# Kernel optimization log

Measured on AMD Instinct MI355X. Metric: run time of the kernel, lower is better.

Reference implementation:

```python
import jax, jax.numpy as jnp
import numpy as np

# GCK basis vectors: all palindromic, so convolution == correlation for them.
_V = np.array([[1., 1., 1.], [1., -1., 1.], [1., 1., -1.]], dtype=np.float32)


def _lin_combs(kernels):
    """Coefficients c s.t. each 3x3 kernel = sum_k c_k * (v_i outer v_j), k=i*3+j.
    kernels: (O, C, 3, 3) -> (O, C*9), matching torch linCombs layout."""
    O, C = kernels.shape[0], kernels.shape[1]
    basis_flat = jnp.asarray(np.kron(_V, _V))           # (9, 9), symmetric
    basis_inv = jnp.linalg.inv(basis_flat)              # 9x9, tiny
    w = kernels.reshape(O, C, 9)
    comb = jnp.einsum('kl,ocl->ock', basis_inv, w)      # (O, C, 9)
    return comb.reshape(O, C * 9)


def setup_inputs() -> dict:
    key = jax.random.key(0)
    k1, k2 = jax.random.split(key)
    C_in, C_out, D = 16, 32, 1024
    x = jax.random.normal(k1, (C_in, D + 2, D + 2), dtype=jnp.float32)
    kernels = jax.random.normal(k2, (C_out, C_in, 3, 3), dtype=jnp.float32)
    return {"x": x, "kernels": kernels}


def reference(x, kernels):
    V = jnp.asarray(_V, dtype=x.dtype)
    lin = _lin_combs(kernels)                                   # (O, C*9)
    O = kernels.shape[0]
    C, H, W = x.shape
    D = H - 2  # result_dim (square image)
    # rowwise pass: 3-tap 'box' filters along height -> (C, 3, D, W)
    rw = jnp.stack([x[:, :-2, :], x[:, 1:-1, :], x[:, 2:, :]], axis=0)  # (3, C, D, W)
    rw = jnp.einsum('ir,rchw->cihw', V, rw)                              # (C, 3, D, W)
    # colwise pass: 3-tap filters along width -> (C, 3, 3, D, D)
    cw = jnp.stack([rw[..., :-2], rw[..., 1:-1], rw[..., 2:]], axis=0)   # (3, C, 3, D, D)
    cw = jnp.einsum('js,scihw->cijhw', V, cw)                            # (C, 3, 3, D, D)
    # final per-output-channel linear combination of the 9 basis responses
    cw = cw.reshape(C * 9, D * D)
    out = lin @ cw                                                       # (O, D*D)
    return out.reshape(O, D, D)
```

## Files before the change

### kernel.cpp

```cpp
#include <hip/hip_runtime.h>

typedef __attribute__((ext_vector_type(8))) short short8;
typedef __attribute__((ext_vector_type(16))) float f32x16;
typedef __attribute__((ext_vector_type(2))) float f32x2;
typedef __attribute__((ext_vector_type(4))) float f32x4u __attribute__((aligned(4)));
typedef __attribute__((ext_vector_type(2))) unsigned int uint2v;

#define C_INPUT 16
#define C_OUTPUT 32
#define DIM 1024
#define HW 1026
#define CH_STRIDE (HW * HW)
#define TH 16
#define TW 32
#define LDS_ROWS 18
#define LDS_W 34
#define ROW_BYTES (LDS_W * 32)
#define LDS_BYTES (LDS_ROWS * ROW_BYTES)
#define NUNITS (4 * LDS_ROWS * 9)

__device__ __forceinline__ unsigned short f2bf(float f) {
    unsigned int u = __builtin_bit_cast(unsigned int, f);
    u += 0x7fffu + ((u >> 16) & 1u);
    return (unsigned short)(u >> 16);
}

__global__ __launch_bounds__(256, 4)
void gck3x3_mfma_kernel(const float* __restrict__ x,
                        const float* __restrict__ kern,
                        float* __restrict__ out) {
    __shared__ __attribute__((aligned(16))) unsigned char s_x[LDS_BYTES];

    const int tid  = threadIdx.x;
    const int lane = tid & 63;
    const int wv   = tid >> 6;
    const int n    = lane & 31;
    const int hi   = lane >> 5;

    const int bid = blockIdx.x;
    const int swz = (bid & 7) * 256 + (bid >> 3);
    const int bh  = swz >> 5;
    const int bw  = swz & 31;
    const int h0  = bh * TH;
    const int w0  = bw * TW;

    f32x4u vals[3][4];
    #pragma unroll
    for (int k = 0; k < 3; ++k) {
        const int idx = tid + k * 256;
        if (idx < NUNITS) {
            const int c4  = idx / (LDS_ROWS * 9);
            const int rem = idx - c4 * (LDS_ROWS * 9);
            const int row = rem / 9;
            const int wq  = rem - row * 9;
            const int w   = wq * 4;
            const float* base = x + (4 * c4) * CH_STRIDE + (h0 + row) * HW + (w0 + w);
            if (wq < 8) {
                #pragma unroll
                for (int j = 0; j < 4; ++j)
                    vals[k][j] = *(const f32x4u*)(base + j * CH_STRIDE);
            } else {
                #pragma unroll
                for (int j = 0; j < 4; ++j) {
                    f32x2 t2 = *(const f32x2*)(base + j * CH_STRIDE);
                    f32x4u v; v[0] = t2[0]; v[1] = t2[1]; v[2] = 0.f; v[3] = 0.f;
                    vals[k][j] = v;
                }
            }
        }
    }

    #pragma unroll
    for (int k = 0; k < 3; ++k) {
        const int idx = tid + k * 256;
        if (idx < NUNITS) {
            const int c4  = idx / (LDS_ROWS * 9);
            const int rem = idx - c4 * (LDS_ROWS * 9);
            const int row = rem / 9;
            const int wq  = rem - row * 9;
            const int w   = wq * 4;
            const int nv  = (wq < 8) ? 4 : 2;
            #pragma unroll
            for (int p = 0; p < 4; ++p) {
                if (p < nv) {
                    const int pp = w + p;
                    const unsigned int lo  = (unsigned int)f2bf(vals[k][0][p]) |
                                             ((unsigned int)f2bf(vals[k][1][p]) << 16);
                    const unsigned int hi2 = (unsigned int)f2bf(vals[k][2][p]) |
                                             ((unsigned int)f2bf(vals[k][3][p]) << 16);
                    const int s16 = ((c4 >> 1) ^ (pp >> 2) ^ (pp >> 3)) & 1;
                    const int off = row * ROW_BYTES + pp * 32 + s16 * 16 + (c4 & 1) * 8;
                    uint2v t; t.x = lo; t.y = hi2;
                    *(uint2v*)(s_x + off) = t;
                }
            }
        }
    }

    short8 af[3][3];
    {
        const int o = n;
        #pragma unroll
        for (int r = 0; r < 3; ++r) {
            #pragma unroll
            for (int s = 0; s < 3; ++s) {
                short8 v;
                #pragma unroll
                for (int j = 0; j < 8; ++j) {
                    const int c = 8 * hi + j;
                    v[j] = (short)f2bf(kern[o * 144 + c * 9 + r * 3 + s]);
                }
                af[r][s] = v;
            }
        }
    }

    __syncthreads();

    #pragma unroll
    for (int t = 0; t < 4; ++t) {
        const int baserow = wv * 4 + t;
        f32x16 acc;
        #pragma unroll
        for (int q = 0; q < 16; ++q) acc[q] = 0.0f;

        #pragma unroll
        for (int r = 0; r < 3; ++r) {
            #pragma unroll
            for (int s = 0; s < 3; ++s) {
                const int w   = n + s;
                const int s16 = (hi ^ (w >> 2) ^ (w >> 3)) & 1;
                const int off = (baserow + r) * ROW_BYTES + w * 32 + s16 * 16;
                const short8 bfr = *(const short8*)(s_x + off);
                acc = __builtin_amdgcn_mfma_f32_32x32x16_bf16(af[r][s], bfr, acc, 0, 0, 0);
            }
        }

        const int h = h0 + baserow;
        #pragma unroll
        for (int q = 0; q < 16; ++q) {
            const int o = (q & 3) + 8 * (q >> 2) + 4 * hi;
            __builtin_nontemporal_store(acc[q], out + (o << 20) + (h << 10) + (w0 + n));
        }
    }
}

extern "C" void kernel_launch(void* const* d_in, const int* in_sizes, int n_in,
                              void* d_out, int out_size, void* d_ws, size_t ws_size,
                              hipStream_t stream) {
    (void)in_sizes; (void)n_in; (void)d_ws; (void)ws_size; (void)out_size;
    const float* x    = (const float*)d_in[0];
    const float* kern = (const float*)d_in[1];
    float*       out  = (float*)d_out;
    gck3x3_mfma_kernel<<<2048, 256, 0, stream>>>(x, kern, out);
}
```

Before: 43.09 us.

## Process two row tiles per block with double-buffered LDS and prefetch overlap

```diff
diff --git a/kernel.cpp b/kernel.cpp
--- a/kernel.cpp
+++ b/kernel.cpp
@@ -3,21 +3,18 @@
 typedef __attribute__((ext_vector_type(8))) short short8;
 typedef __attribute__((ext_vector_type(16))) float f32x16;
 typedef __attribute__((ext_vector_type(2))) float f32x2;
-typedef __attribute__((ext_vector_type(4))) float f32x4u __attribute__((aligned(4)));
+typedef __attribute__((ext_vector_type(4))) float f32x4;
 typedef __attribute__((ext_vector_type(2))) unsigned int uint2v;
 
-#define C_INPUT 16
-#define C_OUTPUT 32
-#define DIM 1024
 #define HW 1026
 #define CH_STRIDE (HW * HW)
 #define TH 16
 #define TW 32
 #define LDS_ROWS 18
-#define LDS_W 34
-#define ROW_BYTES (LDS_W * 32)
-#define LDS_BYTES (LDS_ROWS * ROW_BYTES)
-#define NUNITS (4 * LDS_ROWS * 9)
+#define ROW_BYTES 1120
+#define TILE_BYTES (LDS_ROWS * ROW_BYTES)
+#define UNITS_PER_C4 (LDS_ROWS * 17)
+#define NUNITS (4 * UNITS_PER_C4)
 
 __device__ __forceinline__ unsigned short f2bf(float f) {
     unsigned int u = __builtin_bit_cast(unsigned int, f);
@@ -25,105 +22,60 @@
     return (unsigned short)(u >> 16);
 }
 
-__global__ __launch_bounds__(256, 4)
-void gck3x3_mfma_kernel(const float* __restrict__ x,
-                        const float* __restrict__ kern,
-                        float* __restrict__ out) {
-    __shared__ __attribute__((aligned(16))) unsigned char s_x[LDS_BYTES];
-
-    const int tid  = threadIdx.x;
-    const int lane = tid & 63;
-    const int wv   = tid >> 6;
-    const int n    = lane & 31;
-    const int hi   = lane >> 5;
-
-    const int bid = blockIdx.x;
-    const int swz = (bid & 7) * 256 + (bid >> 3);
-    const int bh  = swz >> 5;
-    const int bw  = swz & 31;
-    const int h0  = bh * TH;
-    const int w0  = bw * TW;
-
-    f32x4u vals[3][4];
+__device__ __forceinline__ void stage_issue(const float* __restrict__ x, int h0, int w0,
+                                            int tid, f32x2 (&vals)[5][4]) {
     #pragma unroll
-    for (int k = 0; k < 3; ++k) {
+    for (int k = 0; k < 5; ++k) {
         const int idx = tid + k * 256;
         if (idx < NUNITS) {
-            const int c4  = idx / (LDS_ROWS * 9);
-            const int rem = idx - c4 * (LDS_ROWS * 9);
-            const int row = rem / 9;
-            const int wq  = rem - row * 9;
-            const int w   = wq * 4;
-            const float* base = x + (4 * c4) * CH_STRIDE + (h0 + row) * HW + (w0 + w);
-            if (wq < 8) {
-                #pragma unroll
-                for (int j = 0; j < 4; ++j)
-                    vals[k][j] = *(const f32x4u*)(base + j * CH_STRIDE);
-            } else {
-                #pragma unroll
-                for (int j = 0; j < 4; ++j) {
-                    f32x2 t2 = *(const f32x2*)(base + j * CH_STRIDE);
-                    f32x4u v; v[0] = t2[0]; v[1] = t2[1]; v[2] = 0.f; v[3] = 0.f;
-                    vals[k][j] = v;
-                }
+            const int c4  = idx / UNITS_PER_C4;
+            const int rem = idx - c4 * UNITS_PER_C4;
+            const int row = rem / 17;
+            const int u   = rem - row * 17;
+            const float* base = x + (4 * c4) * CH_STRIDE + (h0 + row) * HW + (w0 + 2 * u);
+            #pragma unroll
+            for (int j = 0; j < 4; ++j)
+                vals[k][j] = *(const f32x2*)(base + j * CH_STRIDE);
+        }
+    }
+}
+
+__device__ __forceinline__ void stage_write(unsigned char* buf, int tid,
+                                            const f32x2 (&vals)[5][4]) {
+    #pragma unroll
+    for (int k = 0; k < 5; ++k) {
+        const int idx = tid + k * 256;
+        if (idx < NUNITS) {
+            const int c4  = idx / UNITS_PER_C4;
+            const int rem = idx - c4 * UNITS_PER_C4;
+            const int row = rem / 17;
+            const int u   = rem - row * 17;
+            #pragma unroll
+            for (int p = 0; p < 2; ++p) {
+                const int pp = 2 * u + p;
+                const unsigned int lo  = (unsigned int)f2bf(vals[k][0][p]) |
+                                         ((unsigned int)f2bf(vals[k][1][p]) << 16);
+                const unsigned int hi2 = (unsigned int)f2bf(vals[k][2][p]) |
+                                         ((unsigned int)f2bf(vals[k][3][p]) << 16);
+                const int s16 = ((c4 >> 1) ^ (pp >> 2) ^ (pp >> 3)) & 1;
+                const int off = row * ROW_BYTES + pp * 32 + s16 * 16 + (c4 & 1) * 8;
+                uint2v t; t.x = lo; t.y = hi2;
+                *(uint2v*)(buf + off) = t;
             }
         }
     }
+}
 
-    #pragma unroll
-    for (int k = 0; k < 3; ++k) {
-        const int idx = tid + k * 256;
-        if (idx < NUNITS) {
-            const int c4  = idx / (LDS_ROWS * 9);
-            const int rem = idx - c4 * (LDS_ROWS * 9);
-            const int row = rem / 9;
-            const int wq  = rem - row * 9;
-            const int w   = wq * 4;
-            const int nv  = (wq < 8) ? 4 : 2;
-            #pragma unroll
-            for (int p = 0; p < 4; ++p) {
-                if (p < nv) {
-                    const int pp = w + p;
-                    const unsigned int lo  = (unsigned int)f2bf(vals[k][0][p]) |
-                                             ((unsigned int)f2bf(vals[k][1][p]) << 16);
-                    const unsigned int hi2 = (unsigned int)f2bf(vals[k][2][p]) |
-                                             ((unsigned int)f2bf(vals[k][3][p]) << 16);
-                    const int s16 = ((c4 >> 1) ^ (pp >> 2) ^ (pp >> 3)) & 1;
-                    const int off = row * ROW_BYTES + pp * 32 + s16 * 16 + (c4 & 1) * 8;
-                    uint2v t; t.x = lo; t.y = hi2;
-                    *(uint2v*)(s_x + off) = t;
-                }
-            }
-        }
-    }
-
-    short8 af[3][3];
-    {
-        const int o = n;
-        #pragma unroll
-        for (int r = 0; r < 3; ++r) {
-            #pragma unroll
-            for (int s = 0; s < 3; ++s) {
-                short8 v;
-                #pragma unroll
-                for (int j = 0; j < 8; ++j) {
-                    const int c = 8 * hi + j;
-                    v[j] = (short)f2bf(kern[o * 144 + c * 9 + r * 3 + s]);
-                }
-                af[r][s] = v;
-            }
-        }
-    }
-
-    __syncthreads();
-
+__device__ __forceinline__ void compute_store(const unsigned char* buf,
+                                              const short8 (&af)[3][3],
+                                              float* __restrict__ out,
+                                              int h0, int w0, int wv, int n, int hi) {
     #pragma unroll
     for (int t = 0; t < 4; ++t) {
         const int baserow = wv * 4 + t;
         f32x16 acc;
         #pragma unroll
         for (int q = 0; q < 16; ++q) acc[q] = 0.0f;
-
         #pragma unroll
         for (int r = 0; r < 3; ++r) {
             #pragma unroll
@@ -131,11 +83,10 @@
                 const int w   = n + s;
                 const int s16 = (hi ^ (w >> 2) ^ (w >> 3)) & 1;
                 const int off = (baserow + r) * ROW_BYTES + w * 32 + s16 * 16;
-                const short8 bfr = *(const short8*)(s_x + off);
+                const short8 bfr = *(const short8*)(buf + off);
                 acc = __builtin_amdgcn_mfma_f32_32x32x16_bf16(af[r][s], bfr, acc, 0, 0, 0);
             }
         }
-
         const int h = h0 + baserow;
         #pragma unroll
         for (int q = 0; q < 16; ++q) {
@@ -145,6 +96,63 @@
     }
 }
 
+__global__ __launch_bounds__(256, 4)
+void gck3x3_mfma_kernel(const float* __restrict__ x,
+                        const float* __restrict__ kern,
+                        float* __restrict__ out) {
+    __shared__ __attribute__((aligned(16))) unsigned char s_x[2][TILE_BYTES];
+
+    const int tid  = threadIdx.x;
+    const int lane = tid & 63;
+    const int wv   = tid >> 6;
+    const int n    = lane & 31;
+    const int hi   = lane >> 5;
+
+    const int bid = blockIdx.x;
+    const int swz = (bid & 7) * 128 + (bid >> 3);
+    const int ph  = swz >> 5;
+    const int pw  = swz & 31;
+    const int w0  = pw * TW;
+    const int h0a = ph * 32;
+    const int h0b = h0a + TH;
+
+    f32x2 vals[5][4];
+
+    stage_issue(x, h0a, w0, tid, vals);
+
+    short8 af[3][3];
+    {
+        float chunk[72];
+        const float* kbase = kern + n * 144 + hi * 72;
+        #pragma unroll
+        for (int j4 = 0; j4 < 18; ++j4)
+            *(f32x4*)(chunk + 4 * j4) = *(const f32x4*)(kbase + 4 * j4);
+        #pragma unroll
+        for (int r = 0; r < 3; ++r)
+            #pragma unroll
+            for (int s = 0; s < 3; ++s) {
+                short8 v;
+                #pragma unroll
+                for (int j = 0; j < 8; ++j)
+                    v[j] = (short)f2bf(chunk[j * 9 + r * 3 + s]);
+                af[r][s] = v;
+            }
+    }
+
+    stage_write(&s_x[0][0], tid, vals);
+    __syncthreads();
+
+    stage_issue(x, h0b, w0, tid, vals);
+    __builtin_amdgcn_sched_barrier(0);
+
+    compute_store(&s_x[0][0], af, out, h0a, w0, wv, n, hi);
+
+    stage_write(&s_x[1][0], tid, vals);
+    __syncthreads();
+
+    compute_store(&s_x[1][0], af, out, h0b, w0, wv, n, hi);
+}
+
 extern "C" void kernel_launch(void* const* d_in, const int* in_sizes, int n_in,
                               void* d_out, int out_size, void* d_ws, size_t ws_size,
                               hipStream_t stream) {
@@ -152,5 +160,5 @@
     const float* x    = (const float*)d_in[0];
     const float* kern = (const float*)d_in[1];
     float*       out  = (float*)d_out;
-    gck3x3_mfma_kernel<<<2048, 256, 0, stream>>>(x, kern, out);
+    gck3x3_mfma_kernel<<<1024, 256, 0, stream>>>(x, kern, out);
 }
```

Measured after the change: 63.38 us. 1.47x slower.
